# Performance work log

Hardware: AMD Instinct MI355X
Metric: run time of the kernel (lower is better)

The kernel has to match this reference:

```python
import jax, jax.numpy as jnp
import numpy as np

N_NODES = 100000
N_EDGES = 1600000
D = 32            # d_v = d_e = d_g = 32
LATENT = 32
IN_FEAT = 3 * D   # nodes + received-edge agg + globals
OUT_FEAT = 32


def setup_inputs() -> dict:
    key = jax.random.key(0)
    ks = jax.random.split(key, 8)
    node_attr = jax.random.normal(ks[0], (N_NODES, D), dtype=jnp.float32)
    edge_index = jax.random.randint(ks[1], (2, N_EDGES), 0, N_NODES, dtype=jnp.int64)
    edge_attr = jax.random.normal(ks[2], (N_EDGES, D), dtype=jnp.float32)
    global_attr = jax.random.normal(ks[3], (1, D), dtype=jnp.float32)
    W1 = jax.random.normal(ks[4], (IN_FEAT, LATENT), dtype=jnp.float32) * (1.0 / np.sqrt(IN_FEAT))
    b1 = jnp.zeros((LATENT,), dtype=jnp.float32)
    W2 = jax.random.normal(ks[5], (LATENT, OUT_FEAT), dtype=jnp.float32) * (1.0 / np.sqrt(LATENT))
    b2 = jnp.zeros((OUT_FEAT,), dtype=jnp.float32)
    return {"node_attr": node_attr, "edge_index": edge_index, "edge_attr": edge_attr,
            "global_attr": global_attr, "W1": W1, "b1": b1, "W2": W2, "b2": b2}


def reference(node_attr, edge_index, edge_attr, global_attr, W1, b1, W2, b2):
    receivers = edge_index[1]
    # scatter_add of edge features by receiver index -> [N, d_e]
    agg_received = jax.ops.segment_sum(edge_attr, receivers, num_segments=N_NODES)
    # broadcast global attr to all nodes -> [N, d_g]
    g = jnp.broadcast_to(global_attr, (N_NODES, global_attr.shape[1]))
    collected = jnp.concatenate([node_attr, agg_received, g], axis=-1)  # [N, 3d]
    h = jax.nn.relu(collected @ W1 + b1)
    return h @ W2 + b2
```

## Files before the change

kernel.cpp:

```cpp
#include <hip/hip_runtime.h>

#define N_NODES 100000
#define N_EDGES 1600000
#define D 32
#define NB 64
#define K_BUCKETS 1563
#define CAP 1280
#define CHUNK 4096
#define PB 512
#define EPT (CHUNK / PB)
#define PART_BLOCKS 391
#define BINS_PAD 2048
#define CSTRIDE 16
#define NPASS ((CAP + 255) / 256)

__global__ __launch_bounds__(512) void partition_kernel(
    const int* __restrict__ receivers,
    int* __restrict__ cursor,
    unsigned int* __restrict__ slab)
{
    __shared__ int sHist[BINS_PAD];
    __shared__ int sStart[BINS_PAD];
    __shared__ int sCur[BINS_PAD];
    __shared__ int sWs[16];

    const int tid = threadIdx.x;
    const int base = blockIdx.x * CHUNK;
    const int nrem = N_EDGES - base;

    for (int i = tid; i < BINS_PAD; i += PB) sHist[i] = 0;
    __syncthreads();

    int rv[EPT];
    #pragma unroll
    for (int s = 0; s < EPT; ++s) {
        int idx = s * PB + tid;
        rv[s] = (idx < nrem) ? receivers[base + idx] : -1;
        if (rv[s] >= 0) atomicAdd(&sHist[rv[s] >> 6], 1);
    }
    __syncthreads();

    int loc[4];
    int ssum = 0;
    #pragma unroll
    for (int i = 0; i < 4; ++i) {
        int v = sHist[tid * 4 + i];
        loc[i] = ssum;
        ssum += v;
    }
    int inc = ssum;
    #pragma unroll
    for (int off = 1; off < 64; off <<= 1) {
        int y = __shfl_up(inc, off, 64);
        if ((tid & 63) >= off) inc += y;
    }
    const int wave = tid >> 6;
    if ((tid & 63) == 63) sWs[wave] = inc;
    __syncthreads();
    int wbase = 0;
    for (int w = 0; w < wave; ++w) wbase += sWs[w];
    int excl = wbase + inc - ssum;
    #pragma unroll
    for (int i = 0; i < 4; ++i) {
        int e = excl + loc[i];
        sStart[tid * 4 + i] = e;
        sCur[tid * 4 + i] = e;
    }
    __syncthreads();

    for (int k = tid; k < K_BUCKETS; k += PB) {
        int c = sHist[k];
        int g = c ? atomicAdd(&cursor[k * CSTRIDE], c) : 0;
        sHist[k] = g - sStart[k];
    }
    __syncthreads();

    #pragma unroll
    for (int s = 0; s < EPT; ++s) {
        int r = rv[s];
        if (r >= 0) {
            int key = r >> 6;
            int slot = atomicAdd(&sCur[key], 1);
            int pos = sHist[key] + slot;
            if ((unsigned)pos < CAP)
                slab[(size_t)key * CAP + pos] =
                    ((unsigned int)(r & (NB - 1)) << 24) |
                    (unsigned int)(base + s * PB + tid);
        }
    }
}

__global__ __launch_bounds__(256) void fused_kernel(
    const float* __restrict__ node_attr,
    const float* __restrict__ edge_attr,
    const unsigned int* __restrict__ slab,
    const int* __restrict__ cursor,
    const float* __restrict__ gattr,
    const float* __restrict__ W1,
    const float* __restrict__ b1,
    const float* __restrict__ W2,
    const float* __restrict__ b2,
    float* __restrict__ out)
{
    __shared__ float sW1n[1024];
    __shared__ float sW1a[1024];
    __shared__ float sW2[1024];
    __shared__ float sBase[32];
    __shared__ float sB2[32];
    __shared__ float sAgg[NB * 36];
    __shared__ float sH[NB * 36];
    __shared__ unsigned int sSorted[CAP];
    __shared__ int sCnt[NB];
    __shared__ int sStart2[NB];
    __shared__ int sCur2[NB];

    const int tid = threadIdx.x;
    for (int i = tid; i < 1024; i += 256) {
        sW1n[i] = W1[i];
        sW1a[i] = W1[1024 + i];
        sW2[i]  = W2[i];
    }
    if (tid < 32) {
        float acc = b1[tid];
        for (int k = 0; k < 32; ++k) acc += gattr[k] * W1[(64 + k) * 32 + tid];
        sBase[tid] = acc;
        sB2[tid] = b2[tid];
    }
    if (tid < NB) sCnt[tid] = 0;
    __syncthreads();

    const int b = blockIdx.x;
    const int count = min(cursor[b * CSTRIDE], CAP);
    const unsigned int* myslab = slab + (size_t)b * CAP;

    unsigned int pr[NPASS];
    #pragma unroll
    for (int it = 0; it < NPASS; ++it) {
        int i = it * 256 + tid;
        unsigned int p = 0xFFFFFFFFu;
        if (i < count) {
            p = myslab[i];
            atomicAdd(&sCnt[p >> 24], 1);
        }
        pr[it] = p;
    }
    __syncthreads();

    if (tid < 64) {
        int c = sCnt[tid];
        int v = c;
        #pragma unroll
        for (int off = 1; off < 64; off <<= 1) {
            int y = __shfl_up(v, off, 64);
            if (tid >= off) v += y;
        }
        sStart2[tid] = v - c;
        sCur2[tid] = v - c;
    }
    __syncthreads();

    #pragma unroll
    for (int it = 0; it < NPASS; ++it) {
        unsigned int p = pr[it];
        if (p != 0xFFFFFFFFu) {
            int slot = atomicAdd(&sCur2[p >> 24], 1);
            sSorted[slot] = p & 0xFFFFFFu;
        }
    }
    __syncthreads();

    const int g = tid >> 2;
    const int part = tid & 3;
    const int st = sStart2[g];
    const int cn = sCnt[g];

    float a[8];
    #pragma unroll
    for (int jj = 0; jj < 8; ++jj) a[jj] = 0.0f;

    int j = 0;
    for (; j + 3 < cn; j += 4) {
        int e0 = (int)sSorted[st + j];
        int e1 = (int)sSorted[st + j + 1];
        int e2 = (int)sSorted[st + j + 2];
        int e3 = (int)sSorted[st + j + 3];
        const float* r0 = edge_attr + (size_t)e0 * D + part * 8;
        const float* r1 = edge_attr + (size_t)e1 * D + part * 8;
        const float* r2 = edge_attr + (size_t)e2 * D + part * 8;
        const float* r3 = edge_attr + (size_t)e3 * D + part * 8;
        float4 u0 = *(const float4*)(r0);
        float4 u1 = *(const float4*)(r0 + 4);
        float4 v0 = *(const float4*)(r1);
        float4 v1 = *(const float4*)(r1 + 4);
        float4 w0 = *(const float4*)(r2);
        float4 w1 = *(const float4*)(r2 + 4);
        float4 x0 = *(const float4*)(r3);
        float4 x1 = *(const float4*)(r3 + 4);
        a[0] += (u0.x + v0.x) + (w0.x + x0.x);
        a[1] += (u0.y + v0.y) + (w0.y + x0.y);
        a[2] += (u0.z + v0.z) + (w0.z + x0.z);
        a[3] += (u0.w + v0.w) + (w0.w + x0.w);
        a[4] += (u1.x + v1.x) + (w1.x + x1.x);
        a[5] += (u1.y + v1.y) + (w1.y + x1.y);
        a[6] += (u1.z + v1.z) + (w1.z + x1.z);
        a[7] += (u1.w + v1.w) + (w1.w + x1.w);
    }
    for (; j < cn; ++j) {
        int e0 = (int)sSorted[st + j];
        const float* r0 = edge_attr + (size_t)e0 * D + part * 8;
        float4 u0 = *(const float4*)(r0);
        float4 u1 = *(const float4*)(r0 + 4);
        a[0] += u0.x; a[1] += u0.y; a[2] += u0.z; a[3] += u0.w;
        a[4] += u1.x; a[5] += u1.y; a[6] += u1.z; a[7] += u1.w;
    }
    float* dst = &sAgg[g * 36 + part * 8];
    *(float4*)(dst)     = make_float4(a[0], a[1], a[2], a[3]);
    *(float4*)(dst + 4) = make_float4(a[4], a[5], a[6], a[7]);
    __syncthreads();

    const int node = b * NB + g;
    const bool valid = (node < N_NODES);
    const int node_c = valid ? node : (N_NODES - 1);
    const int jb = part * 8;

    float h[8];
    #pragma unroll
    for (int jj = 0; jj < 8; ++jj) h[jj] = sBase[jb + jj];

    const float4* np4 = (const float4*)(node_attr + (size_t)node_c * D);
    #pragma unroll
    for (int q0 = 0; q0 < 8; ++q0) {
        float4 xv = np4[q0];
        float xk[4] = {xv.x, xv.y, xv.z, xv.w};
        #pragma unroll
        for (int kk = 0; kk < 4; ++kk) {
            int k = 4 * q0 + kk;
            float4 w0 = *(const float4*)&sW1n[k * 32 + jb];
            float4 w1 = *(const float4*)&sW1n[k * 32 + jb + 4];
            h[0] += xk[kk] * w0.x; h[1] += xk[kk] * w0.y;
            h[2] += xk[kk] * w0.z; h[3] += xk[kk] * w0.w;
            h[4] += xk[kk] * w1.x; h[5] += xk[kk] * w1.y;
            h[6] += xk[kk] * w1.z; h[7] += xk[kk] * w1.w;
        }
    }
    #pragma unroll 8
    for (int k = 0; k < 32; ++k) {
        float ak = sAgg[g * 36 + k];
        float4 w0 = *(const float4*)&sW1a[k * 32 + jb];
        float4 w1 = *(const float4*)&sW1a[k * 32 + jb + 4];
        h[0] += ak * w0.x; h[1] += ak * w0.y;
        h[2] += ak * w0.z; h[3] += ak * w0.w;
        h[4] += ak * w1.x; h[5] += ak * w1.y;
        h[6] += ak * w1.z; h[7] += ak * w1.w;
    }
    {
        float* hd = &sH[g * 36 + jb];
        #pragma unroll
        for (int jj = 0; jj < 8; ++jj) hd[jj] = fmaxf(h[jj], 0.0f);
    }
    __syncthreads();

    float o[8];
    #pragma unroll
    for (int jj = 0; jj < 8; ++jj) o[jj] = sB2[jb + jj];
    #pragma unroll 8
    for (int k = 0; k < 32; ++k) {
        float hk = sH[g * 36 + k];
        float4 w0 = *(const float4*)&sW2[k * 32 + jb];
        float4 w1 = *(const float4*)&sW2[k * 32 + jb + 4];
        o[0] += hk * w0.x; o[1] += hk * w0.y;
        o[2] += hk * w0.z; o[3] += hk * w0.w;
        o[4] += hk * w1.x; o[5] += hk * w1.y;
        o[6] += hk * w1.z; o[7] += hk * w1.w;
    }

    if (valid) {
        float4* op4 = (float4*)(out + (size_t)node * D + jb);
        op4[0] = make_float4(o[0], o[1], o[2], o[3]);
        op4[1] = make_float4(o[4], o[5], o[6], o[7]);
    }
}

extern "C" void kernel_launch(void* const* d_in, const int* in_sizes, int n_in,
                              void* d_out, int out_size, void* d_ws, size_t ws_size,
                              hipStream_t stream) {
    const float* node_attr  = (const float*)d_in[0];
    const int*   edge_index = (const int*)d_in[1];
    const float* edge_attr  = (const float*)d_in[2];
    const float* gattr      = (const float*)d_in[3];
    const float* W1         = (const float*)d_in[4];
    const float* b1         = (const float*)d_in[5];
    const float* W2         = (const float*)d_in[6];
    const float* b2         = (const float*)d_in[7];
    float* out = (float*)d_out;

    const int* receivers = edge_index + N_EDGES;

    int* cursor = (int*)d_ws;
    unsigned int* slab =
        (unsigned int*)d_ws + (size_t)BINS_PAD * CSTRIDE;

    hipMemsetAsync(cursor, 0, (size_t)BINS_PAD * CSTRIDE * sizeof(int), stream);

    partition_kernel<<<PART_BLOCKS, PB, 0, stream>>>(receivers, cursor, slab);

    fused_kernel<<<K_BUCKETS, 256, 0, stream>>>(
        node_attr, edge_attr, slab, cursor,
        gattr, W1, b1, W2, b2, out);
}
```

Measured before the change: 368.0 us.

## Split fused gather+MLP kernel into separate gather and MLP kernels

Splits the fused kernel in two. The first kernel gathers and sums edge features per receiver bucket and writes the aggregate to a workspace buffer. The second kernel loads that buffer along with the node features and runs the two-layer MLP. The aim is to raise occupancy in the memory-bound gather by dropping the large shared-memory weight buffers from it, at the cost of an extra global write and read of the aggregate (about 12.8 MB each way) and one more kernel launch.

```diff
diff --git a/kernel.cpp b/kernel.cpp
--- a/kernel.cpp
+++ b/kernel.cpp
@@ -14,6 +14,8 @@
 #define CSTRIDE 16
 #define NPASS ((CAP + 255) / 256)
 
+#define AGG_OFF ((size_t)BINS_PAD * CSTRIDE + (size_t)K_BUCKETS * CAP)
+
 __global__ __launch_bounds__(512) void partition_kernel(
     const int* __restrict__ receivers,
     int* __restrict__ cursor,
@@ -90,42 +92,18 @@
     }
 }
 
-__global__ __launch_bounds__(256) void fused_kernel(
-    const float* __restrict__ node_attr,
+__global__ __launch_bounds__(256) void gather_kernel(
     const float* __restrict__ edge_attr,
     const unsigned int* __restrict__ slab,
     const int* __restrict__ cursor,
-    const float* __restrict__ gattr,
-    const float* __restrict__ W1,
-    const float* __restrict__ b1,
-    const float* __restrict__ W2,
-    const float* __restrict__ b2,
-    float* __restrict__ out)
+    float* __restrict__ agg)
 {
-    __shared__ float sW1n[1024];
-    __shared__ float sW1a[1024];
-    __shared__ float sW2[1024];
-    __shared__ float sBase[32];
-    __shared__ float sB2[32];
-    __shared__ float sAgg[NB * 36];
-    __shared__ float sH[NB * 36];
     __shared__ unsigned int sSorted[CAP];
     __shared__ int sCnt[NB];
     __shared__ int sStart2[NB];
     __shared__ int sCur2[NB];
 
     const int tid = threadIdx.x;
-    for (int i = tid; i < 1024; i += 256) {
-        sW1n[i] = W1[i];
-        sW1a[i] = W1[1024 + i];
-        sW2[i]  = W2[i];
-    }
-    if (tid < 32) {
-        float acc = b1[tid];
-        for (int k = 0; k < 32; ++k) acc += gattr[k] * W1[(64 + k) * 32 + tid];
-        sBase[tid] = acc;
-        sB2[tid] = b2[tid];
-    }
     if (tid < NB) sCnt[tid] = 0;
     __syncthreads();
 
@@ -213,11 +191,60 @@
         a[0] += u0.x; a[1] += u0.y; a[2] += u0.z; a[3] += u0.w;
         a[4] += u1.x; a[5] += u1.y; a[6] += u1.z; a[7] += u1.w;
     }
-    float* dst = &sAgg[g * 36 + part * 8];
+
+    float* dst = agg + ((size_t)b * NB + g) * D + part * 8;
     *(float4*)(dst)     = make_float4(a[0], a[1], a[2], a[3]);
     *(float4*)(dst + 4) = make_float4(a[4], a[5], a[6], a[7]);
-    __syncthreads();
-
+}
+
+__global__ __launch_bounds__(256) void mlp_kernel(
+    const float* __restrict__ node_attr,
+    const float* __restrict__ agg,
+    const float* __restrict__ gattr,
+    const float* __restrict__ W1,
+    const float* __restrict__ b1,
+    const float* __restrict__ W2,
+    const float* __restrict__ b2,
+    float* __restrict__ out)
+{
+    __shared__ float sW1n[1024];
+    __shared__ float sW1a[1024];
+    __shared__ float sW2[1024];
+    __shared__ float sBase[32];
+    __shared__ float sB2[32];
+    __shared__ float sAgg[NB * 36];
+    __shared__ float sH[NB * 36];
+
+    const int tid = threadIdx.x;
+    for (int i = tid; i < 1024; i += 256) {
+        sW1n[i] = W1[i];
+        sW1a[i] = W1[1024 + i];
+        sW2[i]  = W2[i];
+    }
+    if (tid < 32) {
+        float acc = b1[tid];
+        for (int k = 0; k < 32; ++k) acc += gattr[k] * W1[(64 + k) * 32 + tid];
+        sBase[tid] = acc;
+        sB2[tid] = b2[tid];
+    }
+
+    const int b = blockIdx.x;
+
+    {
+        const float4* src = (const float4*)(agg + (size_t)b * NB * D);
+        #pragma unroll
+        for (int it = 0; it < 2; ++it) {
+            int i4 = it * 256 + tid;
+            float4 v = src[i4];
+            int nd = i4 >> 3;
+            int of = (i4 & 7) * 4;
+            *(float4*)&sAgg[nd * 36 + of] = v;
+        }
+    }
+    __syncthreads();
+
+    const int g = tid >> 2;
+    const int part = tid & 3;
     const int node = b * NB + g;
     const bool valid = (node < N_NODES);
     const int node_c = valid ? node : (N_NODES - 1);
@@ -299,12 +326,14 @@
     int* cursor = (int*)d_ws;
     unsigned int* slab =
         (unsigned int*)d_ws + (size_t)BINS_PAD * CSTRIDE;
+    float* agg = (float*)d_ws + AGG_OFF;
 
     hipMemsetAsync(cursor, 0, (size_t)BINS_PAD * CSTRIDE * sizeof(int), stream);
 
     partition_kernel<<<PART_BLOCKS, PB, 0, stream>>>(receivers, cursor, slab);
 
-    fused_kernel<<<K_BUCKETS, 256, 0, stream>>>(
-        node_attr, edge_attr, slab, cursor,
-        gattr, W1, b1, W2, b2, out);
+    gather_kernel<<<K_BUCKETS, 256, 0, stream>>>(edge_attr, slab, cursor, agg);
+
+    mlp_kernel<<<K_BUCKETS, 256, 0, stream>>>(
+        node_attr, agg, gattr, W1, b1, W2, b2, out);
 }
```

Measured after the change: 377.1 us. 2.5% more time.
